# Performance work log

Hardware: AMD Instinct MI355X
Metric: run time of the kernel (lower is better)

The kernel has to match this reference:

```python
import jax, jax.numpy as jnp
import numpy as np

B, S, E, H, K = 64, 512, 256, 512, 100


def setup_inputs() -> dict:
    key = jax.random.key(0)
    ks = jax.random.split(key, 7)
    scale = 0.02
    return {
        "event_types": jax.random.randint(ks[0], (B, S), 0, K),
        "time_deltas": jax.random.uniform(ks[1], (B, S), dtype=jnp.float32),
        "embedding": jax.random.normal(ks[2], (K, E), dtype=jnp.float32) * scale,
        "W": jax.random.normal(ks[3], (E + H, 5 * H), dtype=jnp.float32) * scale,
        "b": jnp.zeros((5 * H,), dtype=jnp.float32),
        "Wi": jax.random.normal(ks[4], (H, K), dtype=jnp.float32) * scale,
        "bi": jnp.zeros((K,), dtype=jnp.float32),
    }


def _ctlstm_scan(x_seq, dt_seq, W, b, hidden_dim):
    """x_seq: [B,S,E], dt_seq: [B,S]. Returns h_seq [B,S,H], decay_seq [B,S,H]."""
    bsz = x_seq.shape[0]
    h0 = jnp.zeros((bsz, hidden_dim), x_seq.dtype)
    c0 = jnp.zeros((bsz, hidden_dim), x_seq.dtype)

    def step(carry, inp):
        h, c = carry
        x_t, dt_t = inp  # [B,E], [B]
        z = jnp.concatenate([x_t, h], axis=-1) @ W + b  # [B,5H]
        i, f, o, g, d = jnp.split(z, 5, axis=-1)
        i = jax.nn.sigmoid(i)
        f = jax.nn.sigmoid(f)
        o = jax.nn.sigmoid(o)
        g = jnp.tanh(g)
        decay = jax.nn.softplus(d)  # decay rate >= 0
        c_new = f * c + i * g
        c_t = c_new * jnp.exp(-decay * dt_t[:, None])  # continuous-time decay
        h_t = o * jnp.tanh(c_t)
        return (h_t, c_t), (h_t, decay)

    # time-major for scan
    xs = (jnp.swapaxes(x_seq, 0, 1), jnp.swapaxes(dt_seq, 0, 1))
    _, (h_seq, decay_seq) = jax.lax.scan(step, (h0, c0), xs)
    return jnp.swapaxes(h_seq, 0, 1), jnp.swapaxes(decay_seq, 0, 1)


def reference(event_types, time_deltas, embedding, W, b, Wi, bi):
    x_seq = embedding[event_types]  # [B,S,E]
    hidden_state, decay_rate = _ctlstm_scan(x_seq, time_deltas, W, b, H)
    base_intensities = jax.nn.softplus(hidden_state @ Wi + bi)  # [B,S,K]
    return hidden_state, decay_rate, base_intensities
```

## Files before the change

kernel.cpp:

```cpp
#include <hip/hip_runtime.h>
#include <hip/hip_bf16.h>
#include <stdint.h>

#define BB 64
#define SS 512
#define EE 256
#define HH 512
#define NWG 32

typedef short s16x8 __attribute__((ext_vector_type(8)));
typedef float vf4 __attribute__((ext_vector_type(4)));

#define OFF_WBT   0UL
#define OFF_EMB   3932160UL
#define OFF_WIT   3983360UL
#define OFF_DTT   4098048UL
#define OFF_FLAGS 4229120UL
#define OFF_HBUF  4491264UL
#define OFF_ZXP   38045696UL

__device__ __forceinline__ int fidx(int t, int v, int w) {
  return ((t * 4 + v) << 5) + w;
}

__device__ __forceinline__ unsigned short f2bf(float f) {
  unsigned u = __float_as_uint(f);
  u += 0x7fffu + ((u >> 16) & 1u);
  return (unsigned short)(u >> 16);
}
__device__ __forceinline__ float bf2f(unsigned short h) {
  return __uint_as_float(((unsigned)h) << 16);
}
__device__ __forceinline__ float sigmoidf_(float x) { return 1.f / (1.f + __expf(-x)); }
__device__ __forceinline__ float softplusf_(float x) {
  return fmaxf(x, 0.f) + log1pf(__expf(-fabsf(x)));
}
__device__ __forceinline__ float tanhf_(float x) {
  float e = __expf(2.f * x);
  return 1.f - 2.f / (e + 1.f);
}

__global__ void init_kernel(const float* __restrict__ W, const float* __restrict__ emb,
                            const float* __restrict__ Wi, const float* __restrict__ td,
                            unsigned short* __restrict__ WbT, unsigned short* __restrict__ embB,
                            unsigned short* __restrict__ WiT, float* __restrict__ dtT,
                            int* __restrict__ flags) {
  unsigned i = blockIdx.x * 256u + threadIdx.x;
  if (i < 1966080u) {
    unsigned c = i / 768u, k = i % 768u;
    WbT[i] = f2bf(W[(size_t)k * 2560u + c]);
    return;
  }
  i -= 1966080u;
  if (i < 25600u) { embB[i] = f2bf(emb[i]); return; }
  i -= 25600u;
  if (i < 57344u) {
    unsigned c = i / 512u, k = i % 512u;
    WiT[i] = f2bf(c < 100u ? Wi[(size_t)k * 100u + c] : 0.f);
    return;
  }
  i -= 57344u;
  if (i < 32768u) {
    unsigned t = i / 64u, b = i % 64u;
    dtT[i] = td[(size_t)b * 512u + t];
    return;
  }
  i -= 32768u;
  if (i < 65536u) { flags[i] = 0; return; }
}

__global__ __launch_bounds__(256, 2)
void zx_kernel(const int* __restrict__ evt, const unsigned short* __restrict__ embB,
               const unsigned short* __restrict__ WbT, const float* __restrict__ bias,
               unsigned short* __restrict__ zxp) {
  const int t = blockIdx.y;
  const int tid = threadIdx.x;
  const int v = tid >> 6, lane = tid & 63;
  const int m = lane & 15, quad = lane >> 4;
  const int cbase = blockIdx.x * 256 + v * 64;

  s16x8 Breg[8][4];
#pragma unroll
  for (int cf = 0; cf < 4; ++cf) {
    const unsigned short* bp = WbT + (size_t)(cbase + cf * 16 + m) * 768 + quad * 8;
#pragma unroll
    for (int ch = 0; ch < 8; ++ch) Breg[ch][cf] = *(const s16x8*)(bp + ch * 32);
  }
  int ev[4];
#pragma unroll
  for (int rt = 0; rt < 4; ++rt) ev[rt] = evt[(size_t)(rt * 16 + m) * 512 + t];

  vf4 acc[4][4];
#pragma unroll
  for (int cf = 0; cf < 4; ++cf) {
    float bbv = bias[cbase + cf * 16 + m];
#pragma unroll
    for (int rt = 0; rt < 4; ++rt) acc[rt][cf] = (vf4){bbv, bbv, bbv, bbv};
  }
#pragma unroll
  for (int ch = 0; ch < 8; ++ch) {
#pragma unroll
    for (int rt = 0; rt < 4; ++rt) {
      s16x8 a = *(const s16x8*)(embB + (size_t)ev[rt] * 256 + ch * 32 + quad * 8);
#pragma unroll
      for (int cf = 0; cf < 4; ++cf)
        acc[rt][cf] = __builtin_amdgcn_mfma_f32_16x16x32_bf16(a, Breg[ch][cf], acc[rt][cf], 0, 0, 0);
    }
  }
#pragma unroll
  for (int cf = 0; cf < 4; ++cf) {
    int col0 = cbase + cf * 16;
    int g = col0 >> 9;
    int w = (col0 & 511) >> 4;
#pragma unroll
    for (int rt = 0; rt < 4; ++rt) {
      unsigned h0 = f2bf(acc[rt][cf][0]);
      unsigned h1 = f2bf(acc[rt][cf][1]);
      unsigned h2 = f2bf(acc[rt][cf][2]);
      unsigned h3 = f2bf(acc[rt][cf][3]);
      uint2 val;
      val.x = h0 | (h1 << 16);
      val.y = h2 | (h3 << 16);
      ((uint2*)zxp)[((((size_t)t * 32 + w) * 4 + rt) * 5 + g) * 64 + lane] = val;
    }
  }
}

__global__ __launch_bounds__(256, 1)
void scan_kernel(const unsigned short* __restrict__ WbT,
                 const unsigned short* __restrict__ zxp,
                 const float* __restrict__ dtT,
                 unsigned short* __restrict__ hbuf,
                 int* __restrict__ flags,
                 float* __restrict__ out_h, float* __restrict__ out_d) {
  const int w = blockIdx.x;
  const int tid = threadIdx.x;
  const int v = tid >> 6, lane = tid & 63;
  const int m = lane & 15, quad = lane >> 4;
  const int rowb = v * 16;
  const int bb0 = rowb + quad * 4;
  const int col = w * 16 + m;

  s16x8 Breg[16][5];
#pragma unroll
  for (int g = 0; g < 5; ++g) {
    const unsigned short* bp = WbT + (size_t)(g * 512 + w * 16 + m) * 768 + 256 + quad * 8;
#pragma unroll
    for (int ch = 0; ch < 16; ++ch) Breg[ch][g] = *(const s16x8*)(bp + ch * 32);
  }

  vf4 cst = (vf4){0.f, 0.f, 0.f, 0.f};

  for (int t = 0; t < 512; ++t) {
    vf4 acc[5];
#pragma unroll
    for (int g = 0; g < 5; ++g) {
      uint2 zv = ((const uint2*)zxp)[((((size_t)t * 32 + w) * 4 + v) * 5 + g) * 64 + lane];
      acc[g][0] = bf2f((unsigned short)(zv.x & 0xffffu));
      acc[g][1] = bf2f((unsigned short)(zv.x >> 16));
      acc[g][2] = bf2f((unsigned short)(zv.y & 0xffffu));
      acc[g][3] = bf2f((unsigned short)(zv.y >> 16));
    }
    vf4 dt4 = *(const vf4*)(dtT + t * 64 + bb0);

    if (t > 0) {
      const int tp = t - 1;
      const unsigned short* hsrc =
          hbuf + (size_t)tp * (BB * HH) + (size_t)(rowb + m) * HH + quad * 8;
      const int* fbase = flags + fidx(tp, v, 0);
      unsigned long long done = 0;
      s16x8 areg[16];
#pragma unroll
      for (int ch = 0; ch < 16; ++ch) {
        const unsigned long long need = 3ull << (2 * ch);
        while ((done & need) != need) {
          int f = 0;
          if (lane < 32 && !((done >> lane) & 1ull))
            f = __hip_atomic_load(fbase + lane, __ATOMIC_RELAXED,
                                  __HIP_MEMORY_SCOPE_AGENT);
          done |= __ballot(f != 0);
        }
        __asm__ __volatile__("" ::: "memory");
        areg[ch] = *(const s16x8*)(hsrc + ch * 32);
        if (ch > 0) {
#pragma unroll
          for (int g = 0; g < 5; ++g)
            acc[g] = __builtin_amdgcn_mfma_f32_16x16x32_bf16(areg[ch - 1], Breg[ch - 1][g],
                                                             acc[g], 0, 0, 0);
        }
      }
#pragma unroll
      for (int g = 0; g < 5; ++g)
        acc[g] = __builtin_amdgcn_mfma_f32_16x16x32_bf16(areg[15], Breg[15][g],
                                                         acc[g], 0, 0, 0);
    }

    float hv[4], dv[4];
#pragma unroll
    for (int r = 0; r < 4; ++r) {
      float i_ = sigmoidf_(acc[0][r]);
      float f_ = sigmoidf_(acc[1][r]);
      float o_ = sigmoidf_(acc[2][r]);
      float g_ = tanhf_(acc[3][r]);
      float dec = softplusf_(acc[4][r]);
      float cn = f_ * cst[r] + i_ * g_;
      float ct = cn * __expf(-dec * dt4[r]);
      float h_ = o_ * tanhf_(ct);
      cst[r] = ct;
      hv[r] = h_; dv[r] = dec;
      __hip_atomic_store(hbuf + (size_t)t * (BB * HH) + (size_t)(bb0 + r) * HH + col,
                         f2bf(h_), __ATOMIC_RELAXED, __HIP_MEMORY_SCOPE_AGENT);
    }
    __asm__ __volatile__("" ::: "memory");
    __builtin_amdgcn_s_waitcnt(0);
    __asm__ __volatile__("" ::: "memory");
    if (lane == 0) {
      __hip_atomic_store(flags + fidx(t, v, w), 1, __ATOMIC_RELAXED,
                         __HIP_MEMORY_SCOPE_AGENT);
    }
#pragma unroll
    for (int r = 0; r < 4; ++r) {
      size_t oo = ((size_t)(bb0 + r) * SS + t) * HH + col;
      out_h[oo] = hv[r];
      out_d[oo] = dv[r];
    }
  }
}

__global__ __launch_bounds__(256, 2)
void inten_kernel(const unsigned short* __restrict__ hbuf,
                  const unsigned short* __restrict__ WiT,
                  const float* __restrict__ bi,
                  float* __restrict__ out_i) {
  const int b = blockIdx.y;
  const int t0 = blockIdx.x * 64;
  const int tid = threadIdx.x;
  const int v = tid >> 6, lane = tid & 63;
  const int m = lane & 15, quad = lane >> 4;
  const int trow = t0 + v * 16 + m;

  vf4 acc[7];
#pragma unroll
  for (int cf = 0; cf < 7; ++cf) {
    int c = cf * 16 + m;
    float bbv = (c < 100) ? bi[c] : 0.f;
    acc[cf] = (vf4){bbv, bbv, bbv, bbv};
  }
  const unsigned short* ha = hbuf + ((size_t)trow * 64 + b) * 512 + quad * 8;
#pragma unroll 4
  for (int ch = 0; ch < 16; ++ch) {
    s16x8 a = *(const s16x8*)(ha + ch * 32);
#pragma unroll
    for (int cf = 0; cf < 7; ++cf) {
      s16x8 bf = *(const s16x8*)(WiT + (size_t)(cf * 16 + m) * 512 + ch * 32 + quad * 8);
      acc[cf] = __builtin_amdgcn_mfma_f32_16x16x32_bf16(a, bf, acc[cf], 0, 0, 0);
    }
  }
#pragma unroll
  for (int cf = 0; cf < 7; ++cf) {
    int c = cf * 16 + m;
#pragma unroll
    for (int r = 0; r < 4; ++r) {
      int tt = t0 + v * 16 + quad * 4 + r;
      if (c < 100) out_i[((size_t)b * 512 + tt) * 100 + c] = softplusf_(acc[cf][r]);
    }
  }
}

extern "C" void kernel_launch(void* const* d_in, const int* in_sizes, int n_in,
                              void* d_out, int out_size, void* d_ws, size_t ws_size,
                              hipStream_t stream) {
  (void)in_sizes; (void)n_in; (void)out_size; (void)ws_size;
  const int*   evt  = (const int*)d_in[0];
  const float* td   = (const float*)d_in[1];
  const float* emb  = (const float*)d_in[2];
  const float* W    = (const float*)d_in[3];
  const float* bias = (const float*)d_in[4];
  const float* Wi   = (const float*)d_in[5];
  const float* bi   = (const float*)d_in[6];

  char* ws = (char*)d_ws;
  unsigned short* WbT  = (unsigned short*)(ws + OFF_WBT);
  unsigned short* embB = (unsigned short*)(ws + OFF_EMB);
  unsigned short* WiT  = (unsigned short*)(ws + OFF_WIT);
  float*          dtT  = (float*)(ws + OFF_DTT);
  int*            flags= (int*)(ws + OFF_FLAGS);
  unsigned short* hbuf = (unsigned short*)(ws + OFF_HBUF);
  unsigned short* zxp  = (unsigned short*)(ws + OFF_ZXP);

  float* out_h = (float*)d_out;
  float* out_d = out_h + (size_t)BB * SS * HH;
  float* out_i = out_d + (size_t)BB * SS * HH;

  init_kernel<<<8388, 256, 0, stream>>>(W, emb, Wi, td, WbT, embB, WiT, dtT, flags);
  zx_kernel<<<dim3(10, 512), 256, 0, stream>>>(evt, embB, WbT, bias, zxp);
  scan_kernel<<<NWG, 256, 0, stream>>>(WbT, zxp, dtT, hbuf, flags, out_h, out_d);
  inten_kernel<<<dim3(8, 64), 256, 0, stream>>>(hbuf, WiT, bi, out_i);
}
```

Measured before the change: 3.707 ms.

## Prefetch next-step input projections and wait on all flags before loading h

Result: slower. 4.287 ms (+15.6%).

```diff
diff --git a/kernel.cpp b/kernel.cpp
--- a/kernel.cpp
+++ b/kernel.cpp
@@ -151,48 +151,50 @@
 
   vf4 cst = (vf4){0.f, 0.f, 0.f, 0.f};
 
+  const uint2* zxpu = (const uint2*)zxp;
+  const size_t zoff = (size_t)(w * 4 + v) * 320 + lane;
+  uint2 zxq[5];
+  vf4 dtq;
+#pragma unroll
+  for (int g = 0; g < 5; ++g) zxq[g] = zxpu[zoff + g * 64];
+  dtq = *(const vf4*)(dtT + bb0);
+
   for (int t = 0; t < 512; ++t) {
+    if (t > 0) {
+      const int* fbase = flags + fidx(t - 1, v, 0);
+      unsigned long long done = 0;
+      while ((done & 0xffffffffull) != 0xffffffffull) {
+        int f = 0;
+        if (lane < 32 && !((done >> lane) & 1ull))
+          f = __hip_atomic_load(fbase + lane, __ATOMIC_RELAXED,
+                                __HIP_MEMORY_SCOPE_AGENT);
+        done |= __ballot(f != 0);
+      }
+      __asm__ __volatile__("" ::: "memory");
+    }
+
     vf4 acc[5];
 #pragma unroll
     for (int g = 0; g < 5; ++g) {
-      uint2 zv = ((const uint2*)zxp)[((((size_t)t * 32 + w) * 4 + v) * 5 + g) * 64 + lane];
-      acc[g][0] = bf2f((unsigned short)(zv.x & 0xffffu));
-      acc[g][1] = bf2f((unsigned short)(zv.x >> 16));
-      acc[g][2] = bf2f((unsigned short)(zv.y & 0xffffu));
-      acc[g][3] = bf2f((unsigned short)(zv.y >> 16));
-    }
-    vf4 dt4 = *(const vf4*)(dtT + t * 64 + bb0);
+      acc[g][0] = bf2f((unsigned short)(zxq[g].x & 0xffffu));
+      acc[g][1] = bf2f((unsigned short)(zxq[g].x >> 16));
+      acc[g][2] = bf2f((unsigned short)(zxq[g].y & 0xffffu));
+      acc[g][3] = bf2f((unsigned short)(zxq[g].y >> 16));
+    }
+    vf4 dt4 = dtq;
 
     if (t > 0) {
-      const int tp = t - 1;
       const unsigned short* hsrc =
-          hbuf + (size_t)tp * (BB * HH) + (size_t)(rowb + m) * HH + quad * 8;
-      const int* fbase = flags + fidx(tp, v, 0);
-      unsigned long long done = 0;
+          hbuf + (size_t)(t - 1) * (BB * HH) + (size_t)(rowb + m) * HH + quad * 8;
       s16x8 areg[16];
 #pragma unroll
+      for (int ch = 0; ch < 16; ++ch) areg[ch] = *(const s16x8*)(hsrc + ch * 32);
+#pragma unroll
       for (int ch = 0; ch < 16; ++ch) {
-        const unsigned long long need = 3ull << (2 * ch);
-        while ((done & need) != need) {
-          int f = 0;
-          if (lane < 32 && !((done >> lane) & 1ull))
-            f = __hip_atomic_load(fbase + lane, __ATOMIC_RELAXED,
-                                  __HIP_MEMORY_SCOPE_AGENT);
-          done |= __ballot(f != 0);
-        }
-        __asm__ __volatile__("" ::: "memory");
-        areg[ch] = *(const s16x8*)(hsrc + ch * 32);
-        if (ch > 0) {
-#pragma unroll
-          for (int g = 0; g < 5; ++g)
-            acc[g] = __builtin_amdgcn_mfma_f32_16x16x32_bf16(areg[ch - 1], Breg[ch - 1][g],
-                                                             acc[g], 0, 0, 0);
-        }
+#pragma unroll
+        for (int g = 0; g < 5; ++g)
+          acc[g] = __builtin_amdgcn_mfma_f32_16x16x32_bf16(areg[ch], Breg[ch][g], acc[g], 0, 0, 0);
       }
-#pragma unroll
-      for (int g = 0; g < 5; ++g)
-        acc[g] = __builtin_amdgcn_mfma_f32_16x16x32_bf16(areg[15], Breg[15][g],
-                                                         acc[g], 0, 0, 0);
     }
 
     float hv[4], dv[4];
@@ -218,6 +220,15 @@
       __hip_atomic_store(flags + fidx(t, v, w), 1, __ATOMIC_RELAXED,
                          __HIP_MEMORY_SCOPE_AGENT);
     }
+    __asm__ __volatile__("" ::: "memory");
+
+    if (t < 511) {
+      const uint2* zp = zxpu + (size_t)(t + 1) * 40960 + zoff;
+#pragma unroll
+      for (int g = 0; g < 5; ++g) zxq[g] = zp[g * 64];
+      dtq = *(const vf4*)(dtT + (t + 1) * 64 + bb0);
+    }
+
 #pragma unroll
     for (int r = 0; r < 4; ++r) {
       size_t oo = ((size_t)(bb0 + r) * SS + t) * HH + col;
```
